# Optimization experiments

Measured on AMD Instinct MI355X. Metric: run time of the kernel, lower is better.

## Reference

```python
import jax, jax.numpy as jnp
import numpy as np

B, F, L, H, D = 8, 256, 1024, 4, 256   # batch, filters, seq_len, n_head(=dilation), d_qkv
MODEL = H * F                          # = H * D = 1024
WIN = 128                              # local_window_size


def _local_mask():
    m = np.ones((L, L), dtype=bool)
    m = np.tril(m, WIN - 1)
    m = np.triu(m, -(WIN - 1))
    return jnp.asarray(m)


def setup_inputs() -> dict:
    key = jax.random.key(0)
    ks = jax.random.split(key, 12)
    s = lambda n: 1.0 / np.sqrt(n)
    xav = np.sqrt(6.0 / (L + L))
    return {
        "x": jax.random.normal(ks[0], (B, F, L, H), jnp.float32),
        "Wq_w": jax.random.normal(ks[1], (D, F), jnp.float32) * s(F),
        "Wq_b": jnp.zeros((D,), jnp.float32),
        "Wk_w": jax.random.normal(ks[2], (D, F), jnp.float32) * s(F),
        "Wk_b": jnp.zeros((D,), jnp.float32),
        "Wv_w": jax.random.normal(ks[3], (D, F), jnp.float32) * s(F),
        "Wv_b": jnp.zeros((D,), jnp.float32),
        "w_bias": jax.random.uniform(ks[4], (L, L), jnp.float32, -xav, xav),
        "out_w": jax.random.normal(ks[5], (H * D, MODEL), jnp.float32) * s(H * D),
        "out_b": jnp.zeros((MODEL,), jnp.float32),
        "ln_g": jnp.ones((MODEL,), jnp.float32),
        "ln_b": jnp.zeros((MODEL,), jnp.float32),
        "local_mask": _local_mask(),
    }


def _flatten(y):
    # N C L H -> N L (H C): H outer, C inner in the flattened dim
    n = y.shape[0]
    return y.transpose(0, 2, 3, 1).reshape(n, L, -1)


def reference(x, Wq_w, Wq_b, Wk_w, Wk_b, Wv_w, Wv_b, w_bias, out_w, out_b, ln_g, ln_b, local_mask):
    def proj(w, b):
        # 1x1 Conv2d over (L,H) == channel matmul
        y = jnp.einsum('nclh,dc->ndlh', x, w) + b[None, :, None, None]
        return _flatten(y)

    q = proj(Wq_w, Wq_b)   # [B, L, H*D]
    k = proj(Wk_w, Wk_b)
    v = proj(Wv_w, Wv_b)

    wb = w_bias * local_mask.astype(w_bias.dtype)  # masked bias (masked entries -> 0, exp -> 1)
    ew = jnp.exp(wb)                                # [L, L]
    ek = jnp.exp(k)                                 # [B, L, H*D]
    num = jnp.einsum('ts,nsd->ntd', ew, ek * v)
    den = jnp.einsum('ts,nsd->ntd', ew, ek)
    y = jax.nn.sigmoid(q) * num / den               # [B, L, H*D]

    h = y @ out_w + out_b + _flatten(x)             # residual with flattened input
    mu = jnp.mean(h, axis=-1, keepdims=True)
    var = jnp.mean(jnp.square(h - mu), axis=-1, keepdims=True)
    return (h - mu) * jax.lax.rsqrt(var + 1e-5) * ln_g + ln_b
```

## Files before the change

kernel.cpp:

```cpp
#include <hip/hip_runtime.h>


typedef __attribute__((ext_vector_type(8))) short short8;
typedef __attribute__((ext_vector_type(4))) float f32x4;

#define MBYTE 1048576L

__device__ __forceinline__ unsigned short f2bf(float f) {
  unsigned u = __float_as_uint(f);
  unsigned r = (u + 0x7fff + ((u >> 16) & 1)) >> 16;
  return (unsigned short)r;
}
__device__ __forceinline__ float bf2f(unsigned short s) {
  return __uint_as_float(((unsigned)s) << 16);
}

__global__ void prep_weights(const float* __restrict__ Wq, const float* __restrict__ bq,
                             const float* __restrict__ Wk, const float* __restrict__ bk,
                             const float* __restrict__ Wv, const float* __restrict__ bv,
                             unsigned short* __restrict__ Btp, float* __restrict__ biascat) {
  int i = blockIdx.x * 256 + threadIdx.x;
  int r = i >> 8, c = i & 255;
  const float* W = (r < 256) ? Wq : ((r < 512) ? Wk : Wv);
  int rr = r & 255;
  Btp[i] = f2bf(W[rr * 256 + c]);
  if (c == 0) {
    const float* bp = (r < 256) ? bq : ((r < 512) ? bk : bv);
    biascat[r] = bp[rr];
  }
}

__global__ void prep_ewm1(const float* __restrict__ wbias, unsigned short* __restrict__ ewm1) {
  int i = blockIdx.x * 256 + threadIdx.x;
  int t = i >> 10, s = i & 1023;
  int d = t - s;
  float v = (d >= -127 && d <= 127) ? expm1f(wbias[i]) : 0.0f;
  ewm1[i] = f2bf(v);
}

__global__ void prep_outwT(const float* __restrict__ outw, unsigned short* __restrict__ outwT) {
  __shared__ float tle[32][33];
  int j0 = blockIdx.y * 32, m0 = blockIdx.x * 32;
  int tx = threadIdx.x;
  for (int r = threadIdx.y; r < 32; r += 8)
    tle[r][tx] = outw[(long)(j0 + r) * 1024 + m0 + tx];
  __syncthreads();
  for (int r = threadIdx.y; r < 32; r += 8)
    outwT[(long)(m0 + r) * 1024 + j0 + tx] = f2bf(tle[tx][r]);
}

__global__ void zero_S(float* __restrict__ S) {
  S[blockIdx.x * 256 + threadIdx.x] = 0.0f;
}

__global__ void transpose_x(const float* __restrict__ x, unsigned short* __restrict__ xT) {
  __shared__ float tle[32][33];
  int n = blockIdx.z;
  int c0 = blockIdx.y * 32, lh0 = blockIdx.x * 32;
  int tx = threadIdx.x;
  for (int r = threadIdx.y; r < 32; r += 8)
    tle[r][tx] = x[(long)n * 1048576 + (long)(c0 + r) * 4096 + lh0 + tx];
  __syncthreads();
  for (int r = threadIdx.y; r < 32; r += 8) {
    int lh = lh0 + r, c = c0 + tx;
    int l = lh >> 2, h = lh & 3;
    xT[(long)n * 1048576 + (long)l * 1024 + h * 256 + c] = f2bf(tle[tx][r]);
  }
}

__global__ void transpose_ekv(const unsigned short* __restrict__ ekF,
                              const unsigned short* __restrict__ vF,
                              unsigned short* __restrict__ ekkT,
                              float* __restrict__ S) {
  __shared__ unsigned short tEK[32][33];
  __shared__ unsigned short tEKV[32][33];
  __shared__ float red[2][8][32];
  int n = blockIdx.z;
  int l0 = blockIdx.y * 32, j0 = blockIdx.x * 32;
  int tx = threadIdx.x, ty = threadIdx.y;
  for (int r = ty; r < 32; r += 8) {
    long idx = (long)n * 1048576 + (long)(l0 + r) * 1024 + j0 + tx;
    unsigned short e = ekF[idx];
    unsigned short v = vF[idx];
    tEK[r][tx] = e;
    tEKV[r][tx] = f2bf(bf2f(e) * bf2f(v));
  }
  __syncthreads();
  for (int r = ty; r < 32; r += 8) {
    int j = j0 + r, l = l0 + tx;
    ekkT[(long)n * 2097152 + (long)j * 1024 + l] = tEK[tx][r];
    ekkT[(long)n * 2097152 + (long)(1024 + j) * 1024 + l] = tEKV[tx][r];
  }
  float p0 = 0.f, p1 = 0.f;
#pragma unroll
  for (int q = 0; q < 4; q++) {
    p0 += bf2f(tEK[ty + q * 8][tx]);
    p1 += bf2f(tEKV[ty + q * 8][tx]);
  }
  red[0][ty][tx] = p0;
  red[1][ty][tx] = p1;
  __syncthreads();
  if (ty == 0) {
    float s0 = 0.f, s1 = 0.f;
#pragma unroll
    for (int q = 0; q < 8; q++) {
      s0 += red[0][q][tx];
      s1 += red[1][q][tx];
    }
    atomicAdd(&S[n * 2048 + j0 + tx], s0);
    atomicAdd(&S[n * 2048 + 1024 + j0 + tx], s1);
  }
}

template <int EPI>
__device__ __forceinline__ void gemm_body(
    int bx, int by, int z,
    const unsigned short* __restrict__ A, const unsigned short* __restrict__ Bt,
    int K, int lda, int ldb, long aBatch, long bBatch,
    const float* __restrict__ biascat,
    unsigned short* __restrict__ sq, unsigned short* __restrict__ ekF,
    unsigned short* __restrict__ vF,
    unsigned short* __restrict__ denB, unsigned short* __restrict__ numB,
    const float* __restrict__ Ssum,
    const float* __restrict__ outb, const unsigned short* __restrict__ xTr,
    float* __restrict__ hbuf) {
  __shared__ unsigned short As[128 * 64];
  __shared__ unsigned short Bs[128 * 64];
  const unsigned short* Ab = A + (long)z * aBatch;
  const unsigned short* Bb = Bt + (long)z * bBatch;
  const int m0 = by * 128, n0 = bx * 128;
  const int t = threadIdx.x, lane = t & 63;
  const int wrow = ((t >> 6) >> 1) * 64, wcol = ((t >> 6) & 1) * 64;

  f32x4 zero = {0.f, 0.f, 0.f, 0.f};
  f32x4 acc[4][4];
#pragma unroll
  for (int a = 0; a < 4; a++)
#pragma unroll
    for (int b = 0; b < 4; b++) acc[a][b] = zero;

  int ktLo = 0, ktHi = (K >> 6) - 1;
  if constexpr (EPI == 2) {
    int sLo = m0 - 127; if (sLo < 0) sLo = 0;
    int sHi = m0 + 254; if (sHi > 1023) sHi = 1023;
    ktLo = sLo >> 6;
    ktHi = sHi >> 6;
  }
  for (int kt = ktLo; kt <= ktHi; ++kt) {
    const int k0 = kt << 6;
#pragma unroll
    for (int i = 0; i < 4; i++) {
      const int e = (t + i * 256) * 8;
      const int r = e >> 6, kc = e & 63;
      __builtin_amdgcn_global_load_lds(
          (const __attribute__((address_space(1))) void*)(Ab + (long)(m0 + r) * lda + k0 + kc),
          (__attribute__((address_space(3))) void*)(As + e), 16, 0, 0);
    }
#pragma unroll
    for (int i = 0; i < 4; i++) {
      const int e = (t + i * 256) * 8;
      const int r = e >> 6, kc = e & 63;
      __builtin_amdgcn_global_load_lds(
          (const __attribute__((address_space(1))) void*)(Bb + (long)(n0 + r) * ldb + k0 + kc),
          (__attribute__((address_space(3))) void*)(Bs + e), 16, 0, 0);
    }
    __syncthreads();
#pragma unroll
    for (int ks = 0; ks < 2; ++ks) {
      short8 af[4], bfv[4];
      const int kk = ks * 32 + (lane >> 4) * 8;
#pragma unroll
      for (int fm = 0; fm < 4; fm++)
        af[fm] = *(const short8*)&As[(wrow + fm * 16 + (lane & 15)) * 64 + kk];
#pragma unroll
      for (int fn = 0; fn < 4; fn++)
        bfv[fn] = *(const short8*)&Bs[(wcol + fn * 16 + (lane & 15)) * 64 + kk];
#pragma unroll
      for (int fm = 0; fm < 4; fm++)
#pragma unroll
        for (int fn = 0; fn < 4; fn++)
          acc[fm][fn] =
              __builtin_amdgcn_mfma_f32_16x16x32_bf16(af[fm], bfv[fn], acc[fm][fn], 0, 0, 0);
    }
    __syncthreads();
  }

#pragma unroll
  for (int fm = 0; fm < 4; fm++) {
#pragma unroll
    for (int fn = 0; fn < 4; fn++) {
#pragma unroll
      for (int j = 0; j < 4; j++) {
        const int row = m0 + wrow + fm * 16 + ((lane >> 4) * 4 + j);
        const int col = n0 + wcol + fn * 16 + (lane & 15);
        float val = acc[fm][fn][j];
        if constexpr (EPI == 1) {
          val += biascat[col];
          const int n = row >> 12, l = (row >> 2) & 1023, h = row & 3;
          const long base = (long)n * 1048576 + (long)l * 1024 + h * 256;
          if (col < 256)
            sq[base + col] = f2bf(1.0f / (1.0f + __expf(-val)));
          else if (col < 512)
            ekF[base + (col - 256)] = f2bf(__expf(val));
          else
            vF[base + (col - 512)] = f2bf(val);
        } else if constexpr (EPI == 2) {
          val += Ssum[z * 2048 + col];
          const long base = (long)z * 1048576 + (long)row * 1024;
          if (col < 1024)
            denB[base + col] = f2bf(val);
          else
            numB[base + (col - 1024)] = f2bf(val);
        } else {
          const long idx = (long)row * 1024 + col;
          hbuf[idx] = val + outb[col] + bf2f(xTr[idx]);
        }
      }
    }
  }
}

__global__ __launch_bounds__(256, 2) void gemm1_qkv(
    const unsigned short* __restrict__ A, const unsigned short* __restrict__ Bt,
    const float* __restrict__ biascat,
    unsigned short* __restrict__ sq, unsigned short* __restrict__ ekF,
    unsigned short* __restrict__ vF) {
  int bid = blockIdx.x + 6 * blockIdx.y;
  int c = bid & 7, q = bid >> 3;
  int bx = q % 6, by = c + 8 * (q / 6);
  gemm_body<1>(bx, by, 0, A, Bt, 256, 256, 256, 0L, 0L,
               biascat, sq, ekF, vF, nullptr, nullptr, nullptr, nullptr, nullptr, nullptr);
}

__global__ __launch_bounds__(256, 2) void gemm2_attn(
    const unsigned short* __restrict__ A, const unsigned short* __restrict__ Bt,
    unsigned short* __restrict__ denB, unsigned short* __restrict__ numB,
    const float* __restrict__ Ssum) {
  gemm_body<2>(blockIdx.x, blockIdx.y, blockIdx.z, A, Bt, 1024, 1024, 1024, 0L, 2097152L,
               nullptr, nullptr, nullptr, nullptr, denB, numB, Ssum, nullptr, nullptr, nullptr);
}

__global__ __launch_bounds__(256, 2) void gemm3_out(
    const unsigned short* __restrict__ A, const unsigned short* __restrict__ Bt,
    const float* __restrict__ outb, const unsigned short* __restrict__ xTr,
    float* __restrict__ hbuf) {
  int bid = blockIdx.x + 8 * blockIdx.y;
  int c = bid & 7, q = bid >> 3;
  int bx = q & 7, by = 8 * c + (q >> 3);
  gemm_body<3>(bx, by, 0, A, Bt, 1024, 1024, 1024, 0L, 0L,
               nullptr, nullptr, nullptr, nullptr, nullptr, nullptr, nullptr, outb, xTr, hbuf);
}

__global__ void combine_y(const unsigned short* __restrict__ sq,
                          const unsigned short* __restrict__ denB,
                          const unsigned short* __restrict__ numB,
                          unsigned short* __restrict__ y) {
  const long i = (long)(blockIdx.x * 256 + threadIdx.x) * 4;
  ushort4 s = *(const ushort4*)(sq + i);
  ushort4 d = *(const ushort4*)(denB + i);
  ushort4 nu = *(const ushort4*)(numB + i);
  ushort4 r;
  r.x = f2bf(bf2f(s.x) * bf2f(nu.x) / bf2f(d.x));
  r.y = f2bf(bf2f(s.y) * bf2f(nu.y) / bf2f(d.y));
  r.z = f2bf(bf2f(s.z) * bf2f(nu.z) / bf2f(d.z));
  r.w = f2bf(bf2f(s.w) * bf2f(nu.w) / bf2f(d.w));
  *(ushort4*)(y + i) = r;
}

__global__ __launch_bounds__(256) void ln_k(const float* __restrict__ hbuf,
                                            const float* __restrict__ g,
                                            const float* __restrict__ bb,
                                            float* __restrict__ out) {
  __shared__ float red[16];
  const int row = blockIdx.x, t = threadIdx.x;
  const float4 hv = *(const float4*)(hbuf + (long)row * 1024 + t * 4);
  float s = hv.x + hv.y + hv.z + hv.w;
  float ss = hv.x * hv.x + hv.y * hv.y + hv.z * hv.z + hv.w * hv.w;
#pragma unroll
  for (int off = 32; off > 0; off >>= 1) {
    s += __shfl_down(s, off, 64);
    ss += __shfl_down(ss, off, 64);
  }
  const int wid = t >> 6;
  if ((t & 63) == 0) {
    red[wid] = s;
    red[8 + wid] = ss;
  }
  __syncthreads();
  const float tot = red[0] + red[1] + red[2] + red[3];
  const float tss = red[8] + red[9] + red[10] + red[11];
  const float mu = tot * (1.0f / 1024.0f);
  const float var = tss * (1.0f / 1024.0f) - mu * mu;
  const float rs = rsqrtf(var + 1e-5f);
  const float4 gv = *(const float4*)(g + t * 4);
  const float4 bv = *(const float4*)(bb + t * 4);
  float4 o;
  o.x = (hv.x - mu) * rs * gv.x + bv.x;
  o.y = (hv.y - mu) * rs * gv.y + bv.y;
  o.z = (hv.z - mu) * rs * gv.z + bv.z;
  o.w = (hv.w - mu) * rs * gv.w + bv.w;
  *(float4*)(out + (long)row * 1024 + t * 4) = o;
}

extern "C" void kernel_launch(void* const* d_in, const int* in_sizes, int n_in,
                              void* d_out, int out_size, void* d_ws, size_t ws_size,
                              hipStream_t stream) {
  (void)in_sizes; (void)n_in; (void)out_size; (void)ws_size;
  const float* x     = (const float*)d_in[0];
  const float* Wq_w  = (const float*)d_in[1];
  const float* Wq_b  = (const float*)d_in[2];
  const float* Wk_w  = (const float*)d_in[3];
  const float* Wk_b  = (const float*)d_in[4];
  const float* Wv_w  = (const float*)d_in[5];
  const float* Wv_b  = (const float*)d_in[6];
  const float* wbias = (const float*)d_in[7];
  const float* outw  = (const float*)d_in[8];
  const float* outb  = (const float*)d_in[9];
  const float* lng   = (const float*)d_in[10];
  const float* lnb   = (const float*)d_in[11];
  float* out = (float*)d_out;
  char* ws = (char*)d_ws;

  unsigned short* sq   = (unsigned short*)(ws + 0 * MBYTE);
  unsigned short* ekF  = (unsigned short*)(ws + 16 * MBYTE);
  unsigned short* denB = (unsigned short*)(ws + 16 * MBYTE);
  unsigned short* vF   = (unsigned short*)(ws + 32 * MBYTE);
  unsigned short* numB = (unsigned short*)(ws + 32 * MBYTE);
  unsigned short* xT   = (unsigned short*)(ws + 48 * MBYTE);
  unsigned short* ekkT = (unsigned short*)(ws + 64 * MBYTE);
  float* hbuf          = (float*)(ws + 64 * MBYTE);
  unsigned short* y    = (unsigned short*)(ws + 96 * MBYTE);
  unsigned short* Btp  = (unsigned short*)(ws + 112 * MBYTE);
  float* biascat       = (float*)(ws + 112 * MBYTE + 393216);
  unsigned short* outwT= (unsigned short*)(ws + 112 * MBYTE + 397312);
  unsigned short* ewm1 = (unsigned short*)(ws + 112 * MBYTE + 397312 + 2097152);
  float* Ssum          = (float*)(ws + 112 * MBYTE + 397312 + 2 * 2097152);

  prep_weights<<<768, 256, 0, stream>>>(Wq_w, Wq_b, Wk_w, Wk_b, Wv_w, Wv_b, Btp, biascat);
  prep_ewm1<<<4096, 256, 0, stream>>>(wbias, ewm1);
  prep_outwT<<<dim3(32, 32), dim3(32, 8), 0, stream>>>(outw, outwT);
  zero_S<<<64, 256, 0, stream>>>(Ssum);
  transpose_x<<<dim3(128, 8, 8), dim3(32, 8), 0, stream>>>(x, xT);

  gemm1_qkv<<<dim3(6, 256, 1), 256, 0, stream>>>(xT, Btp, biascat, sq, ekF, vF);

  transpose_ekv<<<dim3(32, 32, 8), dim3(32, 8), 0, stream>>>(ekF, vF, ekkT, Ssum);

  gemm2_attn<<<dim3(16, 8, 8), 256, 0, stream>>>(ewm1, ekkT, denB, numB, Ssum);

  combine_y<<<8192, 256, 0, stream>>>(sq, denB, numB, y);

  gemm3_out<<<dim3(8, 64, 1), 256, 0, stream>>>(y, outwT, outb, xT, hbuf);

  ln_k<<<8192, 256, 0, stream>>>(hbuf, lng, lnb, out);
}
```

Measured before the change: 247.0 us.

## Fuse den/num attention GEMMs and sigmoid combine into one kernel

```diff
diff --git a/kernel.cpp b/kernel.cpp
--- a/kernel.cpp
+++ b/kernel.cpp
@@ -114,20 +114,16 @@
 
 template <int EPI>
 __device__ __forceinline__ void gemm_body(
-    int bx, int by, int z,
+    int bx, int by,
     const unsigned short* __restrict__ A, const unsigned short* __restrict__ Bt,
-    int K, int lda, int ldb, long aBatch, long bBatch,
+    int K, int lda, int ldb,
     const float* __restrict__ biascat,
     unsigned short* __restrict__ sq, unsigned short* __restrict__ ekF,
     unsigned short* __restrict__ vF,
-    unsigned short* __restrict__ denB, unsigned short* __restrict__ numB,
-    const float* __restrict__ Ssum,
     const float* __restrict__ outb, const unsigned short* __restrict__ xTr,
     float* __restrict__ hbuf) {
   __shared__ unsigned short As[128 * 64];
   __shared__ unsigned short Bs[128 * 64];
-  const unsigned short* Ab = A + (long)z * aBatch;
-  const unsigned short* Bb = Bt + (long)z * bBatch;
   const int m0 = by * 128, n0 = bx * 128;
   const int t = threadIdx.x, lane = t & 63;
   const int wrow = ((t >> 6) >> 1) * 64, wcol = ((t >> 6) & 1) * 64;
@@ -139,21 +135,15 @@
 #pragma unroll
     for (int b = 0; b < 4; b++) acc[a][b] = zero;
 
-  int ktLo = 0, ktHi = (K >> 6) - 1;
-  if constexpr (EPI == 2) {
-    int sLo = m0 - 127; if (sLo < 0) sLo = 0;
-    int sHi = m0 + 254; if (sHi > 1023) sHi = 1023;
-    ktLo = sLo >> 6;
-    ktHi = sHi >> 6;
-  }
-  for (int kt = ktLo; kt <= ktHi; ++kt) {
+  const int nK = K >> 6;
+  for (int kt = 0; kt < nK; ++kt) {
     const int k0 = kt << 6;
 #pragma unroll
     for (int i = 0; i < 4; i++) {
       const int e = (t + i * 256) * 8;
       const int r = e >> 6, kc = e & 63;
       __builtin_amdgcn_global_load_lds(
-          (const __attribute__((address_space(1))) void*)(Ab + (long)(m0 + r) * lda + k0 + kc),
+          (const __attribute__((address_space(1))) void*)(A + (long)(m0 + r) * lda + k0 + kc),
           (__attribute__((address_space(3))) void*)(As + e), 16, 0, 0);
     }
 #pragma unroll
@@ -161,7 +151,7 @@
       const int e = (t + i * 256) * 8;
       const int r = e >> 6, kc = e & 63;
       __builtin_amdgcn_global_load_lds(
-          (const __attribute__((address_space(1))) void*)(Bb + (long)(n0 + r) * ldb + k0 + kc),
+          (const __attribute__((address_space(1))) void*)(Bt + (long)(n0 + r) * ldb + k0 + kc),
           (__attribute__((address_space(3))) void*)(Bs + e), 16, 0, 0);
     }
     __syncthreads();
@@ -204,13 +194,6 @@
             ekF[base + (col - 256)] = f2bf(__expf(val));
           else
             vF[base + (col - 512)] = f2bf(val);
-        } else if constexpr (EPI == 2) {
-          val += Ssum[z * 2048 + col];
-          const long base = (long)z * 1048576 + (long)row * 1024;
-          if (col < 1024)
-            denB[base + col] = f2bf(val);
-          else
-            numB[base + (col - 1024)] = f2bf(val);
         } else {
           const long idx = (long)row * 1024 + col;
           hbuf[idx] = val + outb[col] + bf2f(xTr[idx]);
@@ -228,16 +211,92 @@
   int bid = blockIdx.x + 6 * blockIdx.y;
   int c = bid & 7, q = bid >> 3;
   int bx = q % 6, by = c + 8 * (q / 6);
-  gemm_body<1>(bx, by, 0, A, Bt, 256, 256, 256, 0L, 0L,
-               biascat, sq, ekF, vF, nullptr, nullptr, nullptr, nullptr, nullptr, nullptr);
+  gemm_body<1>(bx, by, A, Bt, 256, 256, 256,
+               biascat, sq, ekF, vF, nullptr, nullptr, nullptr);
 }
 
 __global__ __launch_bounds__(256, 2) void gemm2_attn(
-    const unsigned short* __restrict__ A, const unsigned short* __restrict__ Bt,
-    unsigned short* __restrict__ denB, unsigned short* __restrict__ numB,
-    const float* __restrict__ Ssum) {
-  gemm_body<2>(blockIdx.x, blockIdx.y, blockIdx.z, A, Bt, 1024, 1024, 1024, 0L, 2097152L,
-               nullptr, nullptr, nullptr, nullptr, denB, numB, Ssum, nullptr, nullptr, nullptr);
+    const unsigned short* __restrict__ ewm1, const unsigned short* __restrict__ ekkT,
+    const unsigned short* __restrict__ sq, const float* __restrict__ Ssum,
+    unsigned short* __restrict__ y) {
+  __shared__ unsigned short As[128 * 64];
+  __shared__ unsigned short Bek[128 * 64];
+  __shared__ unsigned short Bev[128 * 64];
+  const int z = blockIdx.z;
+  const unsigned short* Bb = ekkT + (long)z * 2097152;
+  const int m0 = blockIdx.y * 128, n0 = blockIdx.x * 128;
+  const int t = threadIdx.x, lane = t & 63;
+  const int wrow = ((t >> 6) >> 1) * 64, wcol = ((t >> 6) & 1) * 64;
+
+  f32x4 zero = {0.f, 0.f, 0.f, 0.f};
+  f32x4 accK[4][4], accV[4][4];
+#pragma unroll
+  for (int a = 0; a < 4; a++)
+#pragma unroll
+    for (int b = 0; b < 4; b++) { accK[a][b] = zero; accV[a][b] = zero; }
+
+  int sLo = m0 - 127; if (sLo < 0) sLo = 0;
+  int sHi = m0 + 254; if (sHi > 1023) sHi = 1023;
+  const int ktLo = sLo >> 6, ktHi = sHi >> 6;
+
+  for (int kt = ktLo; kt <= ktHi; ++kt) {
+    const int k0 = kt << 6;
+#pragma unroll
+    for (int i = 0; i < 4; i++) {
+      const int e = (t + i * 256) * 8;
+      const int r = e >> 6, kc = e & 63;
+      __builtin_amdgcn_global_load_lds(
+          (const __attribute__((address_space(1))) void*)(ewm1 + (long)(m0 + r) * 1024 + k0 + kc),
+          (__attribute__((address_space(3))) void*)(As + e), 16, 0, 0);
+      __builtin_amdgcn_global_load_lds(
+          (const __attribute__((address_space(1))) void*)(Bb + (long)(n0 + r) * 1024 + k0 + kc),
+          (__attribute__((address_space(3))) void*)(Bek + e), 16, 0, 0);
+      __builtin_amdgcn_global_load_lds(
+          (const __attribute__((address_space(1))) void*)(Bb + (long)(1024 + n0 + r) * 1024 + k0 + kc),
+          (__attribute__((address_space(3))) void*)(Bev + e), 16, 0, 0);
+    }
+    __syncthreads();
+#pragma unroll
+    for (int ks = 0; ks < 2; ++ks) {
+      short8 af[4], bk[4], bv[4];
+      const int kk = ks * 32 + (lane >> 4) * 8;
+#pragma unroll
+      for (int fm = 0; fm < 4; fm++)
+        af[fm] = *(const short8*)&As[(wrow + fm * 16 + (lane & 15)) * 64 + kk];
+#pragma unroll
+      for (int fn = 0; fn < 4; fn++) {
+        bk[fn] = *(const short8*)&Bek[(wcol + fn * 16 + (lane & 15)) * 64 + kk];
+        bv[fn] = *(const short8*)&Bev[(wcol + fn * 16 + (lane & 15)) * 64 + kk];
+      }
+#pragma unroll
+      for (int fm = 0; fm < 4; fm++)
+#pragma unroll
+        for (int fn = 0; fn < 4; fn++) {
+          accK[fm][fn] =
+              __builtin_amdgcn_mfma_f32_16x16x32_bf16(af[fm], bk[fn], accK[fm][fn], 0, 0, 0);
+          accV[fm][fn] =
+              __builtin_amdgcn_mfma_f32_16x16x32_bf16(af[fm], bv[fn], accV[fm][fn], 0, 0, 0);
+        }
+    }
+    __syncthreads();
+  }
+
+#pragma unroll
+  for (int fm = 0; fm < 4; fm++) {
+#pragma unroll
+    for (int fn = 0; fn < 4; fn++) {
+#pragma unroll
+      for (int j = 0; j < 4; j++) {
+        const int row = m0 + wrow + fm * 16 + ((lane >> 4) * 4 + j);
+        const int col = n0 + wcol + fn * 16 + (lane & 15);
+        const float den = accK[fm][fn][j] + Ssum[z * 2048 + col];
+        const float num = accV[fm][fn][j] + Ssum[z * 2048 + 1024 + col];
+        const long idx = (long)z * 1048576 + (long)row * 1024 + col;
+        const float s = bf2f(sq[idx]);
+        y[idx] = f2bf(s * num / den);
+      }
+    }
+  }
 }
 
 __global__ __launch_bounds__(256, 2) void gemm3_out(
@@ -247,24 +306,8 @@
   int bid = blockIdx.x + 8 * blockIdx.y;
   int c = bid & 7, q = bid >> 3;
   int bx = q & 7, by = 8 * c + (q >> 3);
-  gemm_body<3>(bx, by, 0, A, Bt, 1024, 1024, 1024, 0L, 0L,
-               nullptr, nullptr, nullptr, nullptr, nullptr, nullptr, nullptr, outb, xTr, hbuf);
-}
-
-__global__ void combine_y(const unsigned short* __restrict__ sq,
-                          const unsigned short* __restrict__ denB,
-                          const unsigned short* __restrict__ numB,
-                          unsigned short* __restrict__ y) {
-  const long i = (long)(blockIdx.x * 256 + threadIdx.x) * 4;
-  ushort4 s = *(const ushort4*)(sq + i);
-  ushort4 d = *(const ushort4*)(denB + i);
-  ushort4 nu = *(const ushort4*)(numB + i);
-  ushort4 r;
-  r.x = f2bf(bf2f(s.x) * bf2f(nu.x) / bf2f(d.x));
-  r.y = f2bf(bf2f(s.y) * bf2f(nu.y) / bf2f(d.y));
-  r.z = f2bf(bf2f(s.z) * bf2f(nu.z) / bf2f(d.z));
-  r.w = f2bf(bf2f(s.w) * bf2f(nu.w) / bf2f(d.w));
-  *(ushort4*)(y + i) = r;
+  gemm_body<3>(bx, by, A, Bt, 1024, 1024, 1024,
+               nullptr, nullptr, nullptr, nullptr, outb, xTr, hbuf);
 }
 
 __global__ __launch_bounds__(256) void ln_k(const float* __restrict__ hbuf,
@@ -323,9 +366,7 @@
 
   unsigned short* sq   = (unsigned short*)(ws + 0 * MBYTE);
   unsigned short* ekF  = (unsigned short*)(ws + 16 * MBYTE);
-  unsigned short* denB = (unsigned short*)(ws + 16 * MBYTE);
   unsigned short* vF   = (unsigned short*)(ws + 32 * MBYTE);
-  unsigned short* numB = (unsigned short*)(ws + 32 * MBYTE);
   unsigned short* xT   = (unsigned short*)(ws + 48 * MBYTE);
   unsigned short* ekkT = (unsigned short*)(ws + 64 * MBYTE);
   float* hbuf          = (float*)(ws + 64 * MBYTE);
@@ -346,9 +387,7 @@
 
   transpose_ekv<<<dim3(32, 32, 8), dim3(32, 8), 0, stream>>>(ekF, vF, ekkT, Ssum);
 
-  gemm2_attn<<<dim3(16, 8, 8), 256, 0, stream>>>(ewm1, ekkT, denB, numB, Ssum);
-
-  combine_y<<<8192, 256, 0, stream>>>(sq, denB, numB, y);
+  gemm2_attn<<<dim3(8, 8, 8), 256, 0, stream>>>(ewm1, ekkT, sq, Ssum, y);
 
   gemm3_out<<<dim3(8, 64, 1), 256, 0, stream>>>(y, outwT, outb, xT, hbuf);
 
```

Result: faster. 236.4 us (-4.3%).
